# Performance work log

Measured on AMD Instinct MI355X. Metric: run time of the kernel, lower is better.

Reference implementation:

```python
import jax, jax.numpy as jnp
import numpy as np

EPS = 1e-3  # kernel epsilon used in Performer generalized kernel
B, H, N, D, M = 1, 8, 1024, 64, 128  # batch, heads, seq, dim_heads, nb_features


def _gaussian_orthogonal_matrix(m, d, seed=0):
    # GaussianOrthogonalRandomMatrix with scaling=0: stacked QR blocks, rows
    # rescaled by chi-distributed norms of gaussian d-vectors.
    rng = np.random.default_rng(seed)
    blocks = []
    for _ in range(m // d):
        g = rng.standard_normal((d, d))
        qmat, _ = np.linalg.qr(g)
        blocks.append(qmat.T)
    proj = np.concatenate(blocks, axis=0)  # [m, d], orthonormal rows per block
    mult = np.linalg.norm(rng.standard_normal((m, d)), axis=1)  # chi norms
    return (mult[:, None] * proj).astype(np.float32)


def setup_inputs() -> dict:
    key = jax.random.key(0)
    kq, kk, kv = jax.random.split(key, 3)
    q = jax.random.normal(kq, (B, H, N, D), dtype=jnp.float32)
    k = jax.random.normal(kk, (B, H, N, D), dtype=jnp.float32)
    v = jax.random.normal(kv, (B, H, N, D), dtype=jnp.float32)
    proj = jnp.asarray(_gaussian_orthogonal_matrix(M, D))
    return {"q": q, "k": k, "v": v, "proj": proj}


def _generalized_kernel(x, proj):
    # kernel_fn(relu)( (x / d**0.25) @ proj^T ) + eps
    normalizer = 1.0 / (x.shape[-1] ** 0.25)
    xp = jnp.einsum('bhnd,md->bhnm', x * normalizer, proj)
    return jax.nn.relu(xp) + EPS


def reference(q, k, v, proj):
    qp = _generalized_kernel(q, proj)  # [B,H,N,M]
    kp = _generalized_kernel(k, proj)  # [B,H,N,M]
    # causal linear attention
    k_cumsum = jnp.cumsum(kp, axis=-2)                              # [B,H,N,M]
    context = jnp.einsum('bhnm,bhne->bhnme', kp, v)                 # [B,H,N,M,D]
    context = jnp.cumsum(context, axis=-3)                          # prefix sums over n
    context = context / k_cumsum[..., None]                         # normalize
    out = jnp.einsum('bhnme,bhnm->bhne', context, qp)               # [B,H,N,D]
    return out
```

## Files before the change

### kernel.cpp

```cpp
#include <hip/hip_runtime.h>

static constexpr int H = 8, N = 1024, D = 64, M = 128;
static constexpr float EPS = 1e-3f;
static constexpr float NORM = 0.35355339059327373f;

typedef __attribute__((ext_vector_type(8))) short short8;
typedef __attribute__((ext_vector_type(4))) float f32x4;

__device__ inline unsigned short f2bf(float x) {
    unsigned u = __float_as_uint(x);
    return (unsigned short)((u + 0x7fffu + ((u >> 16) & 1u)) >> 16);
}
__device__ inline float bf2f(unsigned short u) {
    return __uint_as_float(((unsigned)u) << 16);
}
__device__ inline ushort4 pack4(float4 g) {
    return (ushort4){f2bf(g.x), f2bf(g.y), f2bf(g.z), f2bf(g.w)};
}

__global__ __launch_bounds__(512) void k_projg(const float* __restrict__ q,
                                               const float* __restrict__ k,
                                               const float* __restrict__ proj,
                                               const float* __restrict__ v,
                                               unsigned short* __restrict__ qpb,
                                               unsigned short* __restrict__ kpb,
                                               unsigned short* __restrict__ Gpb,
                                               float* __restrict__ kpart) {
    __shared__ __align__(16) short smem[30208];
    short* projb = smem;
    short* xb = smem + 9216;
    short* obuf = smem + 13824;
    short* kpT = smem + 22528;
    short* vT = smem + 27648;
    const int tid = threadIdx.x;
    const int rblk = blockIdx.x;
    const int h = blockIdx.y;
    const int rowbase = h * N + rblk * 32;
    const int lane = tid & 63, wv = tid >> 6;
    const int rt = wv & 3, mh = wv >> 2;
    const int fr = lane & 15, fq = lane >> 4;

    {
        int r = tid >> 4, dq = tid & 15;
        float4 g = *(const float4*)&q[(rowbase + r) * D + dq * 4];
        float4 gk = *(const float4*)&k[(rowbase + r) * D + dq * 4];
        int rv = tid & 31, e4 = (tid >> 5) * 4;
        float4 gv = *(const float4*)&v[(rowbase + rv) * D + e4];
        g.x *= NORM; g.y *= NORM; g.z *= NORM; g.w *= NORM;
        *(ushort4*)&xb[r * 72 + dq * 4] = pack4(g);
        gk.x *= NORM; gk.y *= NORM; gk.z *= NORM; gk.w *= NORM;
        *(ushort4*)&xb[(32 + r) * 72 + dq * 4] = pack4(gk);
        vT[(e4 + 0) * 40 + rv] = (short)f2bf(gv.x);
        vT[(e4 + 1) * 40 + rv] = (short)f2bf(gv.y);
        vT[(e4 + 2) * 40 + rv] = (short)f2bf(gv.z);
        vT[(e4 + 3) * 40 + rv] = (short)f2bf(gv.w);
    }
    for (int i4 = tid; i4 < 2048; i4 += 512) {
        int m = i4 >> 4, dq = i4 & 15;
        *(ushort4*)&projb[m * 72 + dq * 4] = pack4(*(const float4*)&proj[i4 * 4]);
    }
    __syncthreads();

    f32x4 accp[4];
#pragma unroll
    for (int i = 0; i < 4; i++) accp[i] = (f32x4){0.f, 0.f, 0.f, 0.f};
#pragma unroll
    for (int kt = 0; kt < 2; kt++) {
        short8 a = *(const short8*)&xb[(16 * rt + fr) * 72 + kt * 32 + fq * 8];
#pragma unroll
        for (int i = 0; i < 4; i++) {
            const int mt = mh * 4 + i;
            short8 bb = *(const short8*)&projb[(16 * mt + fr) * 72 + kt * 32 + fq * 8];
            accp[i] = __builtin_amdgcn_mfma_f32_16x16x32_bf16(a, bb, accp[i], 0, 0, 0);
        }
    }
#pragma unroll
    for (int i = 0; i < 4; i++) {
        const int mt = mh * 4 + i;
#pragma unroll
        for (int reg = 0; reg < 4; reg++) {
            const int r = 16 * rt + fq * 4 + reg;
            const int m = 16 * mt + fr;
            unsigned short bv = f2bf(fmaxf(accp[i][reg], 0.f) + EPS);
            obuf[r * 136 + m] = (short)bv;
            if (rt >= 2) kpT[m * 40 + (r - 32)] = (short)bv;
        }
    }
    __syncthreads();

    for (int i = tid; i < 1024; i += 512) {
        int r = i >> 4, cu8 = i & 15;
        short8 val = *(const short8*)&obuf[r * 136 + cu8 * 8];
        unsigned short* g = (r < 32) ? &qpb[(rowbase + r) * M + cu8 * 8]
                                     : &kpb[(rowbase + r - 32) * M + cu8 * 8];
        *(short8*)g = val;
    }
    const int gb = h * 32 + rblk;
    if (tid < 128) {
        float ks = 0.f;
#pragma unroll 8
        for (int r = 0; r < 32; r++) ks += bf2f((unsigned short)kpT[tid * 40 + r]);
        kpart[gb * M + tid] = ks;
    }
    __syncthreads();

    f32x4 gacc[4];
#pragma unroll
    for (int et = 0; et < 4; et++) gacc[et] = (f32x4){0.f, 0.f, 0.f, 0.f};
    {
        short8 a = *(const short8*)&kpT[(16 * wv + fr) * 40 + fq * 8];
#pragma unroll
        for (int et = 0; et < 4; et++) {
            short8 bb = *(const short8*)&vT[(16 * et + fr) * 40 + fq * 8];
            gacc[et] = __builtin_amdgcn_mfma_f32_16x16x32_bf16(a, bb, gacc[et], 0, 0, 0);
        }
    }
#pragma unroll
    for (int et = 0; et < 4; et++)
#pragma unroll
        for (int reg = 0; reg < 4; reg++) {
            const int m = 16 * wv + fq * 4 + reg;
            obuf[m * 68 + 16 * et + fr] = (short)f2bf(gacc[et][reg]);
        }
    __syncthreads();
    for (int i = tid; i < 2048; i += 512) {
        int m = i >> 4, e4 = (i & 15) * 4;
        *(ushort4*)&Gpb[(gb * M + m) * D + e4] = *(const ushort4*)&obuf[m * 68 + e4];
    }
}

__global__ __launch_bounds__(256) void k_prefix(const float* __restrict__ kpart,
                                                const unsigned short* __restrict__ Gpb,
                                                float* __restrict__ zpre,
                                                unsigned short* __restrict__ S0pre) {
    const int h = blockIdx.x >> 5, seg = blockIdx.x & 31;
    const int tid = threadIdx.x;
    const int eb = seg * 256 + tid;
    float g[32];
#pragma unroll
    for (int s = 0; s < 32; s++)
        g[s] = bf2f(Gpb[(h * 32 + s) * (M * D) + eb]);
    float a = 0.f;
    unsigned short o[32];
#pragma unroll
    for (int s = 0; s < 32; s++) {
        o[s] = f2bf(a);
        a += g[s];
    }
#pragma unroll
    for (int s = 0; s < 32; s++)
        S0pre[(h * 32 + s) * (M * D) + eb] = o[s];

    if (seg == 0 && tid < 128) {
        float kv[32];
#pragma unroll
        for (int s = 0; s < 32; s++) kv[s] = kpart[(h * 32 + s) * M + tid];
        float z = 0.f;
        float zo[32];
#pragma unroll
        for (int s = 0; s < 32; s++) {
            zo[s] = z;
            z += kv[s];
        }
#pragma unroll
        for (int s = 0; s < 32; s++)
            zpre[(h * 32 + s) * M + tid] = zo[s];
    }
}

__global__ __launch_bounds__(512) void k_attn(const unsigned short* __restrict__ qpb,
                                              const unsigned short* __restrict__ kpb,
                                              const float* __restrict__ zpre,
                                              const unsigned short* __restrict__ S0pre,
                                              const float* __restrict__ v,
                                              float* __restrict__ out) {
    __shared__ __align__(16) short smem[25600];
    short* bufW = smem;
    short* bufK = smem + 4352;
    short* bufQ = smem + 8704;
    short* s0t  = smem + 13056;
    short* vT   = smem + 21760;
    short* bufP = smem + 24320;
    const int tid = threadIdx.x;
    const int b = blockIdx.x;
    const int h = b >> 5, s = b & 31;
    const int rowstart = h * N + s * 32;
    const int lane = tid & 63, wv = tid >> 6;
    const int rt = wv & 1, js = wv >> 1;
    const int fr = lane & 15, fq = lane >> 4;

    const int sj = tid >> 4, smu = tid & 15;
    short8 kpre = *(const short8*)&kpb[(rowstart + sj) * M + smu * 8];
    short8 qpre = *(const short8*)&qpb[(rowstart + sj) * M + smu * 8];
    const int pm = tid >> 2, peb = (tid & 3) * 16;
    const unsigned short* s0src = &S0pre[(h * 32 + s) * (M * D) + pm * D + peb];
    short8 s0a = *(const short8*)&s0src[0];
    short8 s0b = *(const short8*)&s0src[8];
    const int ve4 = (tid & 15) * 4;
    float4 gv = *(const float4*)&v[(rowstart + sj) * D + ve4];
    const float zinit = zpre[(h * 32 + s) * M + (tid >> 2)];

    *(short8*)&bufK[sj * 136 + smu * 8] = kpre;
    *(short8*)&bufQ[sj * 136 + smu * 8] = qpre;
#pragma unroll
    for (int j = 0; j < 8; j++) {
        s0t[(peb + j) * 136 + pm] = s0a[j];
        s0t[(peb + 8 + j) * 136 + pm] = s0b[j];
    }
    vT[(ve4 + 0) * 40 + sj] = (short)f2bf(gv.x);
    vT[(ve4 + 1) * 40 + sj] = (short)f2bf(gv.y);
    vT[(ve4 + 2) * 40 + sj] = (short)f2bf(gv.z);
    vT[(ve4 + 3) * 40 + sj] = (short)f2bf(gv.w);
    __syncthreads();

    {
        const int zm = tid >> 2, qr = tid & 3, r0 = qr * 8;
        float kv[8];
        float part = 0.f;
#pragma unroll
        for (int r = 0; r < 8; r++) {
            kv[r] = bf2f((unsigned short)bufK[(r0 + r) * 136 + zm]);
            part += kv[r];
        }
        float incl = part, t;
        t = __shfl_up(incl, 1, 4); if (qr >= 1) incl += t;
        t = __shfl_up(incl, 2, 4); if (qr >= 2) incl += t;
        t = __shfl_up(incl, 1, 4);
        float z = zinit + ((qr == 0) ? 0.f : t);
#pragma unroll
        for (int r = 0; r < 8; r++) {
            const int rr = r0 + r;
            z += kv[r];
            bufW[rr * 136 + zm] = (short)f2bf(
                bf2f((unsigned short)bufQ[rr * 136 + zm]) *
                __builtin_amdgcn_rcpf(z));
        }
    }
    __syncthreads();

    f32x4 acc2 = (f32x4){0.f, 0.f, 0.f, 0.f};
#pragma unroll
    for (int kt = 0; kt < 4; kt++) {
        short8 a = *(const short8*)&bufW[(16 * rt + fr) * 136 + kt * 32 + fq * 8];
        short8 bb = *(const short8*)&s0t[(16 * js + fr) * 136 + kt * 32 + fq * 8];
        acc2 = __builtin_amdgcn_mfma_f32_16x16x32_bf16(a, bb, acc2, 0, 0, 0);
    }
    if (wv < 4) {
        const int jt = wv >> 1;
        f32x4 acc1 = (f32x4){0.f, 0.f, 0.f, 0.f};
#pragma unroll
        for (int kt = 0; kt < 4; kt++) {
            short8 a = *(const short8*)&bufW[(16 * rt + fr) * 136 + kt * 32 + fq * 8];
            short8 bb = *(const short8*)&bufK[(16 * jt + fr) * 136 + kt * 32 + fq * 8];
            acc1 = __builtin_amdgcn_mfma_f32_16x16x32_bf16(a, bb, acc1, 0, 0, 0);
        }
        const int j = 16 * jt + fr;
#pragma unroll
        for (int reg = 0; reg < 4; reg++) {
            const int nloc = 16 * rt + fq * 4 + reg;
            float val = (j <= nloc) ? acc1[reg] : 0.f;
            bufP[nloc * 40 + j] = (short)f2bf(val);
        }
    }
    __syncthreads();

    {
        short8 a = *(const short8*)&bufP[(16 * rt + fr) * 40 + fq * 8];
        short8 bb = *(const short8*)&vT[(16 * js + fr) * 40 + fq * 8];
        acc2 = __builtin_amdgcn_mfma_f32_16x16x32_bf16(a, bb, acc2, 0, 0, 0);
    }

#pragma unroll
    for (int reg = 0; reg < 4; reg++) {
        out[(rowstart + 16 * rt + fq * 4 + reg) * D + 16 * js + fr] = acc2[reg];
    }
}

extern "C" void kernel_launch(void* const* d_in, const int* in_sizes, int n_in,
                              void* d_out, int out_size, void* d_ws, size_t ws_size,
                              hipStream_t stream) {
    const float* q = (const float*)d_in[0];
    const float* k = (const float*)d_in[1];
    const float* v = (const float*)d_in[2];
    const float* proj = (const float*)d_in[3];
    float* out = (float*)d_out;

    float* ws = (float*)d_ws;
    float* kpart = ws;
    unsigned short* qpb = (unsigned short*)(kpart + H * 32 * M);
    unsigned short* kpb = qpb + H * N * M;
    unsigned short* Gpb = kpb + H * N * M;
    float* zpre = (float*)(Gpb + H * 32 * M * D);
    unsigned short* S0pre = (unsigned short*)(zpre + H * 32 * M);

    k_projg<<<dim3(32, H), 512, 0, stream>>>(q, k, proj, v, qpb, kpb, Gpb,
                                             kpart);
    k_prefix<<<dim3(256), 256, 0, stream>>>(kpart, Gpb, zpre, S0pre);
    k_attn<<<dim3(H * 32), 512, 0, stream>>>(qpb, kpb, zpre, S0pre, v, out);
}
```

Baseline: 75.41 us.

## Fuse prefix and attention kernels with per-head atomic completion flags

```diff
diff --git a/kernel.cpp b/kernel.cpp
--- a/kernel.cpp
+++ b/kernel.cpp
@@ -129,61 +129,65 @@
     }
 }
 
-__global__ __launch_bounds__(256) void k_prefix(const float* __restrict__ kpart,
-                                                const unsigned short* __restrict__ Gpb,
-                                                float* __restrict__ zpre,
-                                                unsigned short* __restrict__ S0pre) {
-    const int h = blockIdx.x >> 5, seg = blockIdx.x & 31;
+__global__ __launch_bounds__(512, 4) void k_mix(
+    const unsigned short* __restrict__ qpb,
+    const unsigned short* __restrict__ kpb,
+    const float* __restrict__ kpart, const unsigned short* __restrict__ Gpb,
+    float* __restrict__ zpre, unsigned short* __restrict__ S0pre,
+    const float* __restrict__ v, float* __restrict__ out,
+    unsigned* __restrict__ done) {
+    __shared__ __align__(16) short smem[25600];
     const int tid = threadIdx.x;
-    const int eb = seg * 256 + tid;
-    float g[32];
-#pragma unroll
-    for (int s = 0; s < 32; s++)
-        g[s] = bf2f(Gpb[(h * 32 + s) * (M * D) + eb]);
-    float a = 0.f;
-    unsigned short o[32];
-#pragma unroll
-    for (int s = 0; s < 32; s++) {
-        o[s] = f2bf(a);
-        a += g[s];
-    }
-#pragma unroll
-    for (int s = 0; s < 32; s++)
-        S0pre[(h * 32 + s) * (M * D) + eb] = o[s];
-
-    if (seg == 0 && tid < 128) {
-        float kv[32];
-#pragma unroll
-        for (int s = 0; s < 32; s++) kv[s] = kpart[(h * 32 + s) * M + tid];
-        float z = 0.f;
-        float zo[32];
+    const int bid = blockIdx.x;
+
+    if (bid < 128) {
+        const int h = bid >> 4, seg = bid & 15;
+        const int eb = seg * 512 + tid;
+        float g[32];
+#pragma unroll
+        for (int s = 0; s < 32; s++)
+            g[s] = bf2f(Gpb[(h * 32 + s) * (M * D) + eb]);
+        float a = 0.f;
+        unsigned short o[32];
 #pragma unroll
         for (int s = 0; s < 32; s++) {
-            zo[s] = z;
-            z += kv[s];
+            o[s] = f2bf(a);
+            a += g[s];
         }
 #pragma unroll
         for (int s = 0; s < 32; s++)
-            zpre[(h * 32 + s) * M + tid] = zo[s];
-    }
-}
-
-__global__ __launch_bounds__(512) void k_attn(const unsigned short* __restrict__ qpb,
-                                              const unsigned short* __restrict__ kpb,
-                                              const float* __restrict__ zpre,
-                                              const unsigned short* __restrict__ S0pre,
-                                              const float* __restrict__ v,
-                                              float* __restrict__ out) {
-    __shared__ __align__(16) short smem[25600];
+            S0pre[(h * 32 + s) * (M * D) + eb] = o[s];
+
+        if (seg == 0 && tid < 128) {
+            float kv[32];
+#pragma unroll
+            for (int s = 0; s < 32; s++) kv[s] = kpart[(h * 32 + s) * M + tid];
+            float z = 0.f;
+            float zo[32];
+#pragma unroll
+            for (int s = 0; s < 32; s++) {
+                zo[s] = z;
+                z += kv[s];
+            }
+#pragma unroll
+            for (int s = 0; s < 32; s++) zpre[(h * 32 + s) * M + tid] = zo[s];
+        }
+        __syncthreads();
+        if (tid == 0) {
+            __threadfence();
+            atomicAdd(&done[h], 1u);
+        }
+        return;
+    }
+
     short* bufW = smem;
     short* bufK = smem + 4352;
     short* bufQ = smem + 8704;
     short* s0t  = smem + 13056;
     short* vT   = smem + 21760;
     short* bufP = smem + 24320;
-    const int tid = threadIdx.x;
-    const int b = blockIdx.x;
-    const int h = b >> 5, s = b & 31;
+    const int ab = bid - 128;
+    const int h = ab >> 5, s = ab & 31;
     const int rowstart = h * N + s * 32;
     const int lane = tid & 63, wv = tid >> 6;
     const int rt = wv & 1, js = wv >> 1;
@@ -192,26 +196,35 @@
     const int sj = tid >> 4, smu = tid & 15;
     short8 kpre = *(const short8*)&kpb[(rowstart + sj) * M + smu * 8];
     short8 qpre = *(const short8*)&qpb[(rowstart + sj) * M + smu * 8];
+    const int ve4 = (tid & 15) * 4;
+    float4 gv = *(const float4*)&v[(rowstart + sj) * D + ve4];
+
+    *(short8*)&bufK[sj * 136 + smu * 8] = kpre;
+    *(short8*)&bufQ[sj * 136 + smu * 8] = qpre;
+    vT[(ve4 + 0) * 40 + sj] = (short)f2bf(gv.x);
+    vT[(ve4 + 1) * 40 + sj] = (short)f2bf(gv.y);
+    vT[(ve4 + 2) * 40 + sj] = (short)f2bf(gv.z);
+    vT[(ve4 + 3) * 40 + sj] = (short)f2bf(gv.w);
+
+    if (tid == 0) {
+        while (__hip_atomic_load(&done[h], __ATOMIC_RELAXED,
+                                 __HIP_MEMORY_SCOPE_AGENT) < 16u) {
+            __builtin_amdgcn_s_sleep(1);
+        }
+        __threadfence();
+    }
+    __syncthreads();
+
     const int pm = tid >> 2, peb = (tid & 3) * 16;
     const unsigned short* s0src = &S0pre[(h * 32 + s) * (M * D) + pm * D + peb];
     short8 s0a = *(const short8*)&s0src[0];
     short8 s0b = *(const short8*)&s0src[8];
-    const int ve4 = (tid & 15) * 4;
-    float4 gv = *(const float4*)&v[(rowstart + sj) * D + ve4];
-    const float zinit = zpre[(h * 32 + s) * M + (tid >> 2)];
-
-    *(short8*)&bufK[sj * 136 + smu * 8] = kpre;
-    *(short8*)&bufQ[sj * 136 + smu * 8] = qpre;
+    const float zinit = zpre[(h * 32 + s) * M + pm];
 #pragma unroll
     for (int j = 0; j < 8; j++) {
         s0t[(peb + j) * 136 + pm] = s0a[j];
         s0t[(peb + 8 + j) * 136 + pm] = s0b[j];
     }
-    vT[(ve4 + 0) * 40 + sj] = (short)f2bf(gv.x);
-    vT[(ve4 + 1) * 40 + sj] = (short)f2bf(gv.y);
-    vT[(ve4 + 2) * 40 + sj] = (short)f2bf(gv.z);
-    vT[(ve4 + 3) * 40 + sj] = (short)f2bf(gv.w);
-    __syncthreads();
 
     {
         const int zm = tid >> 2, qr = tid & 3, r0 = qr * 8;
@@ -285,16 +298,17 @@
     const float* proj = (const float*)d_in[3];
     float* out = (float*)d_out;
 
-    float* ws = (float*)d_ws;
-    float* kpart = ws;
+    unsigned* done = (unsigned*)d_ws;
+    float* kpart = (float*)((char*)d_ws + 64);
     unsigned short* qpb = (unsigned short*)(kpart + H * 32 * M);
     unsigned short* kpb = qpb + H * N * M;
     unsigned short* Gpb = kpb + H * N * M;
     float* zpre = (float*)(Gpb + H * 32 * M * D);
     unsigned short* S0pre = (unsigned short*)(zpre + H * 32 * M);
 
+    hipMemsetAsync(d_ws, 0, 64, stream);
     k_projg<<<dim3(32, H), 512, 0, stream>>>(q, k, proj, v, qpb, kpb, Gpb,
                                              kpart);
-    k_prefix<<<dim3(256), 256, 0, stream>>>(kpart, Gpb, zpre, S0pre);
-    k_attn<<<dim3(H * 32), 512, 0, stream>>>(qpb, kpb, zpre, S0pre, v, out);
-}
+    k_mix<<<dim3(384), 512, 0, stream>>>(qpb, kpb, kpart, Gpb, zpre, S0pre, v,
+                                         out, done);
+}
```

New measurement: 96.12 us. +27.5%, slower.
